# Kernel tuning notes

Measured on AMD Instinct MI355X. Metric: run time of the kernel, lower is better.

## Reference

```python
import jax, jax.numpy as jnp
import numpy as np

E = 20    # number of residue types (rc.restypes)
NB = 2    # num_blocks per AngleHead
NA = 7    # num_angles
C_S = 384
C_H = 128
BS, L = 8, 2048


def setup_inputs() -> dict:
    key = jax.random.key(0)
    ks = jax.random.split(key, 16)
    sc = 0.02
    return {
        "s": jax.random.normal(ks[0], (BS, L, C_S), dtype=jnp.float32),
        "s_init": jax.random.normal(ks[1], (BS, L, C_S), dtype=jnp.float32),
        "aatype": jax.random.randint(ks[2], (BS, L), 0, E, dtype=jnp.int32),
        # stacked per-residue-type AngleHead params
        "Win": jax.random.normal(ks[3], (E, C_S, C_H), dtype=jnp.float32) * sc,
        "b_in": jax.random.normal(ks[4], (E, C_H), dtype=jnp.float32) * sc,
        "Winit": jax.random.normal(ks[5], (E, C_S, C_H), dtype=jnp.float32) * sc,
        "b_init2": jax.random.normal(ks[6], (E, C_H), dtype=jnp.float32) * sc,
        "Wb1": jax.random.normal(ks[7], (E, NB, C_H, C_H), dtype=jnp.float32) * sc,
        "bb1": jax.random.normal(ks[8], (E, NB, C_H), dtype=jnp.float32) * sc,
        "Wb2": jax.random.normal(ks[9], (E, NB, C_H, C_H), dtype=jnp.float32) * sc,
        "bb2": jax.random.normal(ks[10], (E, NB, C_H), dtype=jnp.float32) * sc,
        "Wout": jax.random.normal(ks[11], (E, C_H, NA * 2), dtype=jnp.float32) * sc,
        "b_out": jax.random.normal(ks[12], (E, NA * 2), dtype=jnp.float32) * sc,
    }


def reference(s, s_init, aatype, Win, b_in, Winit, b_init2, Wb1, bb1, Wb2, bb2, Wout, b_out):
    relu = jax.nn.relu
    bs, seq_len, c_s = s.shape
    N = bs * seq_len
    sf = s.reshape(N, c_s)          # [N, c_s]
    si = s_init.reshape(N, c_s)     # [N, c_s]

    # Dense dispatch: run every token through all E per-type heads, then
    # combine with the one-hot routing mask (math identical to the torch
    # gather/scatter loop over residue types).
    h = jnp.einsum('nd,edh->neh', relu(sf), Win) + b_in            # [N,E,H]
    h = h + jnp.einsum('nd,edh->neh', relu(si), Winit) + b_init2   # [N,E,H]

    for b in range(NB):  # ResidualBlock1d: s + W2 @ relu(W1 @ relu(s))
        a = jnp.einsum('neh,ehk->nek', relu(h), Wb1[:, b]) + bb1[:, b]
        a = jnp.einsum('nek,ekh->neh', relu(a), Wb2[:, b]) + bb2[:, b]
        h = h + a

    out = jnp.einsum('neh,eho->neo', relu(h), Wout) + b_out        # [N,E,2*NA]
    sel = jax.nn.one_hot(aatype.reshape(N), E, dtype=out.dtype)    # [N,E]
    ang = jnp.einsum('neo,ne->no', out, sel).reshape(bs, seq_len, NA, 2)

    # F.normalize(dim=-1): x / max(||x||, eps)
    nrm = jnp.maximum(jnp.linalg.norm(ang, axis=-1, keepdims=True), 1e-12)
    return ang / nrm
```

## Files before the change

### kernel.cpp

```cpp
#include <hip/hip_runtime.h>
#include <math.h>

#define E_TYPES 20
#define NBLK 2
#define NANG 7
#define CS 384
#define CH 128
#define N_TOK (8 * 2048)
#define TOK 32
#define TPB 256
#define TPB_MAIN 512
#define KC 128
#define MAX_TILES (N_TOK / TOK + E_TYPES)
#define NPREP 64

#define HIST_OFF 0
#define CNT_OFF 1536
#define POFF_OFF 1600
#define PERM_OFF 2048

#define WT1_OFF (256 * 1024)
#define WT1_SZ  (20 * 8 * 24 * 2048)
#define WTR_OFF (WT1_OFF + WT1_SZ)

typedef __attribute__((ext_vector_type(8))) short bfrag;
typedef __attribute__((ext_vector_type(4))) float f32x4;

__device__ __forceinline__ void split_bf16(float x, unsigned short& h, unsigned short& l) {
    unsigned int u = __float_as_uint(x);
    unsigned int hb = (u + 0x7FFFu + ((u >> 16) & 1u)) & 0xFFFF0000u;
    h = (unsigned short)(hb >> 16);
    float r = x - __uint_as_float(hb);
    unsigned int v = __float_as_uint(r);
    l = (unsigned short)((v + 0x7FFFu + ((v >> 16) & 1u)) >> 16);
}

__global__ void prep1(const float* __restrict__ Win, const float* __restrict__ Winit,
                      const float* __restrict__ Wb1, const float* __restrict__ Wb2,
                      const int* __restrict__ aatype, int* __restrict__ wsI,
                      unsigned short* __restrict__ wt) {
    __shared__ int lh[E_TYPES];
    int bid = blockIdx.x;
    int t = threadIdx.x;
    if (bid >= 1600) {
        int b2 = bid - 1600;
        if (t < E_TYPES) lh[t] = 0;
        __syncthreads();
        int idx = b2 * 256 + t;
        if (idx < N_TOK) atomicAdd(&lh[aatype[idx]], 1);
        __syncthreads();
        if (t < E_TYPES) wsI[HIST_OFF + b2 * E_TYPES + t] = lh[t];
        return;
    }
    int gid = bid * 256 + t;
    unsigned short h[8], l[8];
    if (gid < 245760) {
        int lane = gid & 63;
        int bi = gid >> 6;
        int kb = bi % 24;
        int r = bi / 24;
        int nt = r & 7, e = r >> 3;
        int n = nt * 16 + (lane & 15);
        int k0 = kb * 32 + (lane >> 4) * 8;
        #pragma unroll
        for (int j = 0; j < 8; j++) {
            int k = k0 + j;
            float x = (k < CS) ? Win[((size_t)e * CS + k) * CH + n]
                               : Winit[((size_t)e * CS + (k - CS)) * CH + n];
            split_bf16(x, h[j], l[j]);
        }
        unsigned short* dst = wt + (WT1_OFF / 2) + (size_t)bi * 1024 + lane * 8;
        *(bfrag*)dst = *(bfrag*)h;
        *(bfrag*)(dst + 512) = *(bfrag*)l;
    } else {
        gid -= 245760;
        int lane = gid & 63;
        int bi = gid >> 6;
        int kb = bi & 3;
        int nt = (bi >> 2) & 7;
        int m4 = (bi >> 5) & 3;
        int e = bi >> 7;
        int b = m4 >> 1;
        const float* W = (m4 & 1) ? Wb2 : Wb1;
        int n = nt * 16 + (lane & 15);
        int k0 = kb * 32 + (lane >> 4) * 8;
        #pragma unroll
        for (int j = 0; j < 8; j++) {
            int k = k0 + j;
            float x = W[(((size_t)e * NBLK + b) * CH + k) * CH + n];
            split_bf16(x, h[j], l[j]);
        }
        unsigned short* dst = wt + (WTR_OFF / 2) + (size_t)bi * 1024 + lane * 8;
        *(bfrag*)dst = *(bfrag*)h;
        *(bfrag*)(dst + 512) = *(bfrag*)l;
    }
}

__global__ void scatter_k(const int* __restrict__ aatype, int* ws) {
    __shared__ int lhist[NPREP * E_TYPES];
    __shared__ int counts[E_TYPES], poff[E_TYPES + 1], mybase[E_TYPES], lcur[E_TYPES];
    int t = threadIdx.x;
    int bid = blockIdx.x;
    for (int idx = t; idx < NPREP * E_TYPES; idx += TPB)
        lhist[idx] = ws[HIST_OFF + idx];
    if (t < E_TYPES) lcur[t] = 0;
    __syncthreads();
    if (t < E_TYPES) {
        int tot = 0, pre = 0;
        for (int b = 0; b < NPREP; b++) {
            int v = lhist[b * E_TYPES + t];
            tot += v;
            if (b < bid) pre += v;
        }
        counts[t] = tot;
        mybase[t] = pre;
    }
    __syncthreads();
    if (t == 0) {
        int off = 0;
        for (int e = 0; e < E_TYPES; e++) {
            poff[e] = off;
            off += (counts[e] + TOK - 1) & ~(TOK - 1);
        }
        poff[E_TYPES] = off;
    }
    __syncthreads();
    if (t < E_TYPES) mybase[t] += poff[t];
    __syncthreads();
    int idx = bid * blockDim.x + t;
    if (idx < N_TOK) {
        int e = aatype[idx];
        int r = atomicAdd(&lcur[e], 1);
        ws[PERM_OFF + mybase[e] + r] = idx;
    }
    if (bid == 0) {
        if (t < E_TYPES) ws[CNT_OFF + t] = counts[t];
        if (t == 0)
            for (int e = 0; e <= E_TYPES; e++) ws[POFF_OFF + e] = poff[e];
    }
}

#define MFMA(a, b, c) __builtin_amdgcn_mfma_f32_16x16x32_bf16((a), (b), (c), 0, 0, 0)

__global__ __launch_bounds__(TPB_MAIN)
void angle_main(const float* __restrict__ s, const float* __restrict__ si,
                const float* __restrict__ b_in, const float* __restrict__ b_init2,
                const float* __restrict__ bb1, const float* __restrict__ bb2,
                const float* __restrict__ Wout, const float* __restrict__ b_out,
                const int* __restrict__ wsI, const unsigned short* __restrict__ wt,
                float* __restrict__ out)
{
    __shared__ unsigned short Ah[TOK][136];
    __shared__ unsigned short Al[TOK][136];
    __shared__ float Hf[TOK][132];
    __shared__ float Of[TOK][16];
    __shared__ int ptok[TOK];

    int pos = blockIdx.x * TOK;
    if (pos >= wsI[POFF_OFF + E_TYPES]) return;
    int e = 0;
    while (e < E_TYPES - 1 && pos >= wsI[POFF_OFF + e + 1]) e++;
    int n = wsI[CNT_OFF + e] - (pos - wsI[POFF_OFF + e]);
    if (n > TOK) n = TOK;

    int t = threadIdx.x;
    if (t < TOK) ptok[t] = wsI[PERM_OFF + pos + ((t < n) ? t : 0)];

    int w = t >> 6, lane = t & 63;
    int lane15 = lane & 15, quad = lane >> 4;
    int nc = w * 16 + lane15;

    const bfrag* wt1 = (const bfrag*)((const char*)wt + WT1_OFF);
    const bfrag* wtr = (const bfrag*)((const char*)wt + WTR_OFF);

    f32x4 acc[2];
    {
        float bv = b_in[e * CH + nc] + b_init2[e * CH + nc];
        acc[0] = (f32x4){bv, bv, bv, bv};
        acc[1] = acc[0];
    }

    __syncthreads();

    int srow = t >> 4;
    int scol = (t & 15) * 8;
    size_t rowoff = (size_t)ptok[srow] * CS + scol;
    float4 p0 = *(const float4*)(s + rowoff);
    float4 p1 = *(const float4*)(s + rowoff + 4);

    for (int c = 0; c < 6; c++) {
        {
            float xv[8] = {p0.x, p0.y, p0.z, p0.w, p1.x, p1.y, p1.z, p1.w};
            unsigned short h8[8], l8[8];
            #pragma unroll
            for (int j = 0; j < 8; j++)
                split_bf16(fmaxf(xv[j], 0.f), h8[j], l8[j]);
            *(bfrag*)&Ah[srow][scol] = *(bfrag*)h8;
            *(bfrag*)&Al[srow][scol] = *(bfrag*)l8;
        }
        __syncthreads();
        if (c < 5) {
            const float* src = (c + 1 < 3) ? s : si;
            int kb0 = ((c + 1 < 3) ? (c + 1) : (c - 2)) * KC;
            p0 = *(const float4*)(src + rowoff + kb0);
            p1 = *(const float4*)(src + rowoff + kb0 + 4);
        }
        #pragma unroll
        for (int ks = 0; ks < 4; ks++) {
            int kb = c * 4 + ks;
            int kl = ks * 32 + quad * 8;
            bfrag ah0 = *(const bfrag*)&Ah[lane15][kl];
            bfrag ah1 = *(const bfrag*)&Ah[16 + lane15][kl];
            bfrag al0 = *(const bfrag*)&Al[lane15][kl];
            bfrag al1 = *(const bfrag*)&Al[16 + lane15][kl];
            size_t b0 = ((size_t)(e * 8 + w) * 24 + kb) * 128;
            bfrag bh = wt1[b0 + lane];
            bfrag bl = wt1[b0 + 64 + lane];
            acc[0] = MFMA(ah0, bh, acc[0]);
            acc[0] = MFMA(ah0, bl, acc[0]);
            acc[0] = MFMA(al0, bh, acc[0]);
            acc[1] = MFMA(ah1, bh, acc[1]);
            acc[1] = MFMA(ah1, bl, acc[1]);
            acc[1] = MFMA(al1, bh, acc[1]);
        }
        __syncthreads();
    }

    for (int b = 0; b < NBLK; b++) {
        #pragma unroll
        for (int mt = 0; mt < 2; mt++) {
            f32x4 v = acc[mt];
            #pragma unroll
            for (int r = 0; r < 4; r++) {
                int m = mt * 16 + quad * 4 + r;
                unsigned short hh, ll;
                split_bf16(fmaxf(v[r], 0.f), hh, ll);
                Ah[m][nc] = hh;
                Al[m][nc] = ll;
            }
        }
        __syncthreads();

        f32x4 a2[2];
        {
            float bv = bb1[(e * NBLK + b) * CH + nc];
            a2[0] = (f32x4){bv, bv, bv, bv};
            a2[1] = a2[0];
        }
        #pragma unroll
        for (int ks = 0; ks < 4; ks++) {
            int kl = ks * 32 + quad * 8;
            bfrag ah0 = *(const bfrag*)&Ah[lane15][kl];
            bfrag ah1 = *(const bfrag*)&Ah[16 + lane15][kl];
            bfrag al0 = *(const bfrag*)&Al[lane15][kl];
            bfrag al1 = *(const bfrag*)&Al[16 + lane15][kl];
            size_t b0 = (((size_t)(e * 4 + 2 * b) * 8 + w) * 4 + ks) * 128;
            bfrag bh = wtr[b0 + lane], bl = wtr[b0 + 64 + lane];
            a2[0] = MFMA(ah0, bh, a2[0]);
            a2[0] = MFMA(ah0, bl, a2[0]);
            a2[0] = MFMA(al0, bh, a2[0]);
            a2[1] = MFMA(ah1, bh, a2[1]);
            a2[1] = MFMA(ah1, bl, a2[1]);
            a2[1] = MFMA(al1, bh, a2[1]);
        }
        __syncthreads();

        #pragma unroll
        for (int mt = 0; mt < 2; mt++) {
            f32x4 v = a2[mt];
            #pragma unroll
            for (int r = 0; r < 4; r++) {
                int m = mt * 16 + quad * 4 + r;
                unsigned short hh, ll;
                split_bf16(fmaxf(v[r], 0.f), hh, ll);
                Ah[m][nc] = hh;
                Al[m][nc] = ll;
            }
        }
        __syncthreads();

        f32x4 a3[2];
        {
            float bv = bb2[(e * NBLK + b) * CH + nc];
            a3[0] = (f32x4){bv, bv, bv, bv};
            a3[1] = a3[0];
        }
        #pragma unroll
        for (int ks = 0; ks < 4; ks++) {
            int kl = ks * 32 + quad * 8;
            bfrag ah0 = *(const bfrag*)&Ah[lane15][kl];
            bfrag ah1 = *(const bfrag*)&Ah[16 + lane15][kl];
            bfrag al0 = *(const bfrag*)&Al[lane15][kl];
            bfrag al1 = *(const bfrag*)&Al[16 + lane15][kl];
            size_t b0 = (((size_t)(e * 4 + 2 * b + 1) * 8 + w) * 4 + ks) * 128;
            bfrag bh = wtr[b0 + lane], bl = wtr[b0 + 64 + lane];
            a3[0] = MFMA(ah0, bh, a3[0]);
            a3[0] = MFMA(ah0, bl, a3[0]);
            a3[0] = MFMA(al0, bh, a3[0]);
            a3[1] = MFMA(ah1, bh, a3[1]);
            a3[1] = MFMA(ah1, bl, a3[1]);
            a3[1] = MFMA(al1, bh, a3[1]);
        }
        acc[0] += a3[0];
        acc[1] += a3[1];
        __syncthreads();
    }

    #pragma unroll
    for (int mt = 0; mt < 2; mt++) {
        f32x4 v = acc[mt];
        #pragma unroll
        for (int r = 0; r < 4; r++)
            Hf[mt * 16 + quad * 4 + r][nc] = fmaxf(v[r], 0.f);
    }
    __syncthreads();

    const float* WoutE = Wout + (size_t)e * CH * (NANG * 2);
    const float* boutE = b_out + (size_t)e * (NANG * 2);
    for (int idx = t; idx < n * (NANG * 2); idx += TPB_MAIN) {
        int i = idx / (NANG * 2);
        int o = idx - i * (NANG * 2);
        float v0 = boutE[o], v1 = 0.f, v2 = 0.f, v3 = 0.f;
        #pragma unroll 4
        for (int k = 0; k < CH; k += 4) {
            v0 = fmaf(Hf[i][k],     WoutE[(size_t)k * (NANG * 2) + o],       v0);
            v1 = fmaf(Hf[i][k + 1], WoutE[(size_t)(k + 1) * (NANG * 2) + o], v1);
            v2 = fmaf(Hf[i][k + 2], WoutE[(size_t)(k + 2) * (NANG * 2) + o], v2);
            v3 = fmaf(Hf[i][k + 3], WoutE[(size_t)(k + 3) * (NANG * 2) + o], v3);
        }
        Of[i][o] = (v0 + v1) + (v2 + v3);
    }
    __syncthreads();

    for (int idx = t; idx < n * NANG; idx += TPB_MAIN) {
        int i = idx / NANG;
        int a = idx - i * NANG;
        float x = Of[i][2 * a];
        float y = Of[i][2 * a + 1];
        float nr = fmaxf(sqrtf(x * x + y * y), 1e-12f);
        size_t base = (size_t)ptok[i] * (NANG * 2) + 2 * a;
        out[base]     = x / nr;
        out[base + 1] = y / nr;
    }
}

extern "C" void kernel_launch(void* const* d_in, const int* in_sizes, int n_in,
                              void* d_out, int out_size, void* d_ws, size_t ws_size,
                              hipStream_t stream) {
    const float* s       = (const float*)d_in[0];
    const float* s_init  = (const float*)d_in[1];
    const int*   aatype  = (const int*)d_in[2];
    const float* Win     = (const float*)d_in[3];
    const float* b_in    = (const float*)d_in[4];
    const float* Winit   = (const float*)d_in[5];
    const float* b_init2 = (const float*)d_in[6];
    const float* Wb1     = (const float*)d_in[7];
    const float* bb1     = (const float*)d_in[8];
    const float* Wb2     = (const float*)d_in[9];
    const float* bb2     = (const float*)d_in[10];
    const float* Wout    = (const float*)d_in[11];
    const float* b_out   = (const float*)d_in[12];
    int* wsI = (int*)d_ws;
    unsigned short* wt = (unsigned short*)d_ws;
    float* out = (float*)d_out;

    hipLaunchKernelGGL(prep1, dim3(1664), dim3(256), 0, stream,
                       Win, Winit, Wb1, Wb2, aatype, wsI, wt);
    hipLaunchKernelGGL(scatter_k, dim3(NPREP), dim3(TPB), 0, stream, aatype, wsI);
    hipLaunchKernelGGL(angle_main, dim3(MAX_TILES), dim3(TPB_MAIN), 0, stream,
                       s, s_init, b_in, b_init2, bb1, bb2, Wout, b_out,
                       wsI, wt, out);
}
```

Baseline: 160.0 us.

## Fuse token scatter into main kernel with double-buffered LDS and weight prefetch

Removes the separate scatter kernel. Each main block now rebuilds its tile's token list from the histogram with a wave-level prefix scan over aatype. The LDS activation buffers are double-buffered so one barrier per stage can be dropped, and the next weight fragments are prefetched into registers before they are needed. Block IDs are also remapped for XCD-aware tile assignment. This saves a kernel launch and some barriers, but every block now does redundant histogram and aatype scanning.

New measurement: 155.6 us. 2.8% less time.

```diff
diff --git a/kernel.cpp b/kernel.cpp
--- a/kernel.cpp
+++ b/kernel.cpp
@@ -15,9 +15,6 @@
 #define NPREP 64
 
 #define HIST_OFF 0
-#define CNT_OFF 1536
-#define POFF_OFF 1600
-#define PERM_OFF 2048
 
 #define WT1_OFF (256 * 1024)
 #define WT1_SZ  (20 * 8 * 24 * 2048)
@@ -25,6 +22,7 @@
 
 typedef __attribute__((ext_vector_type(8))) short bfrag;
 typedef __attribute__((ext_vector_type(4))) float f32x4;
+typedef unsigned short (*arr136)[136];
 
 __device__ __forceinline__ void split_bf16(float x, unsigned short& h, unsigned short& l) {
     unsigned int u = __float_as_uint(x);
@@ -96,50 +94,6 @@
     }
 }
 
-__global__ void scatter_k(const int* __restrict__ aatype, int* ws) {
-    __shared__ int lhist[NPREP * E_TYPES];
-    __shared__ int counts[E_TYPES], poff[E_TYPES + 1], mybase[E_TYPES], lcur[E_TYPES];
-    int t = threadIdx.x;
-    int bid = blockIdx.x;
-    for (int idx = t; idx < NPREP * E_TYPES; idx += TPB)
-        lhist[idx] = ws[HIST_OFF + idx];
-    if (t < E_TYPES) lcur[t] = 0;
-    __syncthreads();
-    if (t < E_TYPES) {
-        int tot = 0, pre = 0;
-        for (int b = 0; b < NPREP; b++) {
-            int v = lhist[b * E_TYPES + t];
-            tot += v;
-            if (b < bid) pre += v;
-        }
-        counts[t] = tot;
-        mybase[t] = pre;
-    }
-    __syncthreads();
-    if (t == 0) {
-        int off = 0;
-        for (int e = 0; e < E_TYPES; e++) {
-            poff[e] = off;
-            off += (counts[e] + TOK - 1) & ~(TOK - 1);
-        }
-        poff[E_TYPES] = off;
-    }
-    __syncthreads();
-    if (t < E_TYPES) mybase[t] += poff[t];
-    __syncthreads();
-    int idx = bid * blockDim.x + t;
-    if (idx < N_TOK) {
-        int e = aatype[idx];
-        int r = atomicAdd(&lcur[e], 1);
-        ws[PERM_OFF + mybase[e] + r] = idx;
-    }
-    if (bid == 0) {
-        if (t < E_TYPES) ws[CNT_OFF + t] = counts[t];
-        if (t == 0)
-            for (int e = 0; e <= E_TYPES; e++) ws[POFF_OFF + e] = poff[e];
-    }
-}
-
 #define MFMA(a, b, c) __builtin_amdgcn_mfma_f32_16x16x32_bf16((a), (b), (c), 0, 0, 0)
 
 __global__ __launch_bounds__(TPB_MAIN)
@@ -147,29 +101,88 @@
                 const float* __restrict__ b_in, const float* __restrict__ b_init2,
                 const float* __restrict__ bb1, const float* __restrict__ bb2,
                 const float* __restrict__ Wout, const float* __restrict__ b_out,
+                const int* __restrict__ aatype,
                 const int* __restrict__ wsI, const unsigned short* __restrict__ wt,
                 float* __restrict__ out)
 {
-    __shared__ unsigned short Ah[TOK][136];
-    __shared__ unsigned short Al[TOK][136];
-    __shared__ float Hf[TOK][132];
-    __shared__ float Of[TOK][16];
+    #define BUFSZ 17408
+    __shared__ __align__(16) char pool[2 * BUFSZ];
     __shared__ int ptok[TOK];
-
-    int pos = blockIdx.x * TOK;
-    if (pos >= wsI[POFF_OFF + E_TYPES]) return;
-    int e = 0;
-    while (e < E_TYPES - 1 && pos >= wsI[POFF_OFF + e + 1]) e++;
-    int n = wsI[CNT_OFF + e] - (pos - wsI[POFF_OFF + e]);
-    if (n > TOK) n = TOK;
+    __shared__ int cntS[E_TYPES];
+
+    arr136 AH0 = (arr136)(pool);
+    arr136 AL0 = (arr136)(pool + 8704);
+    arr136 AH1 = (arr136)(pool + BUFSZ);
+    arr136 AL1 = (arr136)(pool + BUFSZ + 8704);
+    float (*Hf)[132] = (float (*)[132])(pool);
+    float (*Of)[16]  = (float (*)[16])(pool + BUFSZ);
 
     int t = threadIdx.x;
-    if (t < TOK) ptok[t] = wsI[PERM_OFF + pos + ((t < n) ? t : 0)];
-
     int w = t >> 6, lane = t & 63;
     int lane15 = lane & 15, quad = lane >> 4;
+
+    int bid = blockIdx.x;
+    const int q = MAX_TILES >> 3, r = MAX_TILES & 7;
+    int xcd = bid & 7, sub = bid >> 3;
+    int tile = (xcd < r ? xcd * (q + 1) : r * (q + 1) + (xcd - r) * q) + sub;
+
+    if (w == 0 && lane < E_TYPES) {
+        int c = 0;
+        #pragma unroll
+        for (int b = 0; b < NPREP; b++) c += wsI[HIST_OFF + b * E_TYPES + lane];
+        cntS[lane] = c;
+    }
+    __syncthreads();
+
+    int pos = tile * TOK;
+    int e = -1, poff_e = 0;
+    {
+        int acc = 0;
+        #pragma unroll
+        for (int ee = 0; ee < E_TYPES; ee++) {
+            int pad = (cntS[ee] + TOK - 1) & ~(TOK - 1);
+            if (e < 0 && pos < acc + pad) { e = ee; poff_e = acc; }
+            acc += pad;
+        }
+        if (pos >= acc) return;
+    }
+    int pos_in = pos - poff_e;
+    int cnt_e = cntS[e];
+    int n = cnt_e - pos_in; if (n > TOK) n = TOK;
+
+    if (w == 0) {
+        int hb = wsI[HIST_OFF + lane * E_TYPES + e];
+        int inc = hb;
+        #pragma unroll
+        for (int d = 1; d < 64; d <<= 1) { int v = __shfl_up(inc, d); if (lane >= d) inc += v; }
+        int pre = inc - hb;
+        unsigned long long mle = __ballot(pre <= pos_in);
+        int cb = 63 - __clzll(mle);
+        int running = __shfl(pre, cb);
+        int base = cb * 256;
+        int lim = pos_in + n;
+        while (running < lim && base < N_TOK) {
+            const int4 a4 = *(const int4*)&aatype[base + lane * 4];
+            int m0 = (a4.x == e), m1 = (a4.y == e), m2 = (a4.z == e), m3 = (a4.w == e);
+            int c = m0 + m1 + m2 + m3;
+            int incl = c;
+            #pragma unroll
+            for (int d = 1; d < 64; d <<= 1) { int v = __shfl_up(incl, d); if (lane >= d) incl += v; }
+            int rk = running + incl - c;
+            int tk = base + lane * 4;
+            if (m0) { if (rk >= pos_in && rk < lim) ptok[rk - pos_in] = tk;     rk++; }
+            if (m1) { if (rk >= pos_in && rk < lim) ptok[rk - pos_in] = tk + 1; rk++; }
+            if (m2) { if (rk >= pos_in && rk < lim) ptok[rk - pos_in] = tk + 2; rk++; }
+            if (m3) { if (rk >= pos_in && rk < lim) ptok[rk - pos_in] = tk + 3; rk++; }
+            running += __shfl(incl, 63);
+            base += 256;
+        }
+        int t0 = ptok[0];
+        if (lane >= n && lane < TOK) ptok[lane] = t0;
+    }
+    __syncthreads();
+
     int nc = w * 16 + lane15;
-
     const bfrag* wt1 = (const bfrag*)((const char*)wt + WT1_OFF);
     const bfrag* wtr = (const bfrag*)((const char*)wt + WTR_OFF);
 
@@ -180,42 +193,45 @@
         acc[1] = acc[0];
     }
 
-    __syncthreads();
-
     int srow = t >> 4;
     int scol = (t & 15) * 8;
     size_t rowoff = (size_t)ptok[srow] * CS + scol;
     float4 p0 = *(const float4*)(s + rowoff);
     float4 p1 = *(const float4*)(s + rowoff + 4);
-
+    size_t wb = (size_t)(e * 8 + w) * 24;
+    bfrag pbh = wt1[wb * 128 + lane];
+    bfrag pbl = wt1[wb * 128 + 64 + lane];
+
+    #pragma unroll
     for (int c = 0; c < 6; c++) {
+        arr136 WAH = (c & 1) ? AH1 : AH0;
+        arr136 WAL = (c & 1) ? AL1 : AL0;
         {
             float xv[8] = {p0.x, p0.y, p0.z, p0.w, p1.x, p1.y, p1.z, p1.w};
             unsigned short h8[8], l8[8];
             #pragma unroll
             for (int j = 0; j < 8; j++)
                 split_bf16(fmaxf(xv[j], 0.f), h8[j], l8[j]);
-            *(bfrag*)&Ah[srow][scol] = *(bfrag*)h8;
-            *(bfrag*)&Al[srow][scol] = *(bfrag*)l8;
-        }
-        __syncthreads();
+            *(bfrag*)&WAH[srow][scol] = *(bfrag*)h8;
+            *(bfrag*)&WAL[srow][scol] = *(bfrag*)l8;
+        }
         if (c < 5) {
             const float* src = (c + 1 < 3) ? s : si;
             int kb0 = ((c + 1 < 3) ? (c + 1) : (c - 2)) * KC;
             p0 = *(const float4*)(src + rowoff + kb0);
             p1 = *(const float4*)(src + rowoff + kb0 + 4);
         }
+        __syncthreads();
         #pragma unroll
         for (int ks = 0; ks < 4; ks++) {
             int kb = c * 4 + ks;
+            bfrag bh = ks ? wt1[(wb + kb) * 128 + lane]      : pbh;
+            bfrag bl = ks ? wt1[(wb + kb) * 128 + 64 + lane] : pbl;
             int kl = ks * 32 + quad * 8;
-            bfrag ah0 = *(const bfrag*)&Ah[lane15][kl];
-            bfrag ah1 = *(const bfrag*)&Ah[16 + lane15][kl];
-            bfrag al0 = *(const bfrag*)&Al[lane15][kl];
-            bfrag al1 = *(const bfrag*)&Al[16 + lane15][kl];
-            size_t b0 = ((size_t)(e * 8 + w) * 24 + kb) * 128;
-            bfrag bh = wt1[b0 + lane];
-            bfrag bl = wt1[b0 + 64 + lane];
+            bfrag ah0 = *(const bfrag*)&WAH[lane15][kl];
+            bfrag ah1 = *(const bfrag*)&WAH[16 + lane15][kl];
+            bfrag al0 = *(const bfrag*)&WAL[lane15][kl];
+            bfrag al1 = *(const bfrag*)&WAL[16 + lane15][kl];
             acc[0] = MFMA(ah0, bh, acc[0]);
             acc[0] = MFMA(ah0, bl, acc[0]);
             acc[0] = MFMA(al0, bh, acc[0]);
@@ -223,95 +239,69 @@
             acc[1] = MFMA(ah1, bl, acc[1]);
             acc[1] = MFMA(al1, bh, acc[1]);
         }
+        if (c < 5) {
+            pbh = wt1[(wb + (c + 1) * 4) * 128 + lane];
+            pbl = wt1[(wb + (c + 1) * 4) * 128 + 64 + lane];
+        }
+    }
+
+    {
+        size_t g0 = ((size_t)(e * 4) * 8 + w) * 4;
+        pbh = wtr[g0 * 128 + lane];
+        pbl = wtr[g0 * 128 + 64 + lane];
+    }
+    f32x4 cur[2] = {acc[0], acc[1]};
+    #pragma unroll
+    for (int g = 0; g < 4; g++) {
+        arr136 WAH = (g & 1) ? AH1 : AH0;
+        arr136 WAL = (g & 1) ? AL1 : AL0;
+        #pragma unroll
+        for (int mt = 0; mt < 2; mt++) {
+            f32x4 v = cur[mt];
+            #pragma unroll
+            for (int rr = 0; rr < 4; rr++) {
+                unsigned short hh, ll;
+                split_bf16(fmaxf(v[rr], 0.f), hh, ll);
+                WAH[mt * 16 + quad * 4 + rr][nc] = hh;
+                WAL[mt * 16 + quad * 4 + rr][nc] = ll;
+            }
+        }
         __syncthreads();
-    }
-
-    for (int b = 0; b < NBLK; b++) {
-        #pragma unroll
-        for (int mt = 0; mt < 2; mt++) {
-            f32x4 v = acc[mt];
-            #pragma unroll
-            for (int r = 0; r < 4; r++) {
-                int m = mt * 16 + quad * 4 + r;
-                unsigned short hh, ll;
-                split_bf16(fmaxf(v[r], 0.f), hh, ll);
-                Ah[m][nc] = hh;
-                Al[m][nc] = ll;
-            }
-        }
-        __syncthreads();
-
-        f32x4 a2[2];
-        {
-            float bv = bb1[(e * NBLK + b) * CH + nc];
-            a2[0] = (f32x4){bv, bv, bv, bv};
-            a2[1] = a2[0];
-        }
+        float bv = (g & 1) ? bb2[(e * NBLK + (g >> 1)) * CH + nc]
+                           : bb1[(e * NBLK + (g >> 1)) * CH + nc];
+        f32x4 r0 = (f32x4){bv, bv, bv, bv}, r1 = r0;
+        size_t wgb = ((size_t)(e * 4 + g) * 8 + w) * 4;
         #pragma unroll
         for (int ks = 0; ks < 4; ks++) {
+            bfrag bh = ks ? wtr[(wgb + ks) * 128 + lane]      : pbh;
+            bfrag bl = ks ? wtr[(wgb + ks) * 128 + 64 + lane] : pbl;
             int kl = ks * 32 + quad * 8;
-            bfrag ah0 = *(const bfrag*)&Ah[lane15][kl];
-            bfrag ah1 = *(const bfrag*)&Ah[16 + lane15][kl];
-            bfrag al0 = *(const bfrag*)&Al[lane15][kl];
-            bfrag al1 = *(const bfrag*)&Al[16 + lane15][kl];
-            size_t b0 = (((size_t)(e * 4 + 2 * b) * 8 + w) * 4 + ks) * 128;
-            bfrag bh = wtr[b0 + lane], bl = wtr[b0 + 64 + lane];
-            a2[0] = MFMA(ah0, bh, a2[0]);
-            a2[0] = MFMA(ah0, bl, a2[0]);
-            a2[0] = MFMA(al0, bh, a2[0]);
-            a2[1] = MFMA(ah1, bh, a2[1]);
-            a2[1] = MFMA(ah1, bl, a2[1]);
-            a2[1] = MFMA(al1, bh, a2[1]);
-        }
-        __syncthreads();
-
-        #pragma unroll
-        for (int mt = 0; mt < 2; mt++) {
-            f32x4 v = a2[mt];
-            #pragma unroll
-            for (int r = 0; r < 4; r++) {
-                int m = mt * 16 + quad * 4 + r;
-                unsigned short hh, ll;
-                split_bf16(fmaxf(v[r], 0.f), hh, ll);
-                Ah[m][nc] = hh;
-                Al[m][nc] = ll;
-            }
-        }
-        __syncthreads();
-
-        f32x4 a3[2];
-        {
-            float bv = bb2[(e * NBLK + b) * CH + nc];
-            a3[0] = (f32x4){bv, bv, bv, bv};
-            a3[1] = a3[0];
-        }
-        #pragma unroll
-        for (int ks = 0; ks < 4; ks++) {
-            int kl = ks * 32 + quad * 8;
-            bfrag ah0 = *(const bfrag*)&Ah[lane15][kl];
-            bfrag ah1 = *(const bfrag*)&Ah[16 + lane15][kl];
-            bfrag al0 = *(const bfrag*)&Al[lane15][kl];
-            bfrag al1 = *(const bfrag*)&Al[16 + lane15][kl];
-            size_t b0 = (((size_t)(e * 4 + 2 * b + 1) * 8 + w) * 4 + ks) * 128;
-            bfrag bh = wtr[b0 + lane], bl = wtr[b0 + 64 + lane];
-            a3[0] = MFMA(ah0, bh, a3[0]);
-            a3[0] = MFMA(ah0, bl, a3[0]);
-            a3[0] = MFMA(al0, bh, a3[0]);
-            a3[1] = MFMA(ah1, bh, a3[1]);
-            a3[1] = MFMA(ah1, bl, a3[1]);
-            a3[1] = MFMA(al1, bh, a3[1]);
-        }
-        acc[0] += a3[0];
-        acc[1] += a3[1];
-        __syncthreads();
+            bfrag ah0 = *(const bfrag*)&WAH[lane15][kl];
+            bfrag ah1 = *(const bfrag*)&WAH[16 + lane15][kl];
+            bfrag al0 = *(const bfrag*)&WAL[lane15][kl];
+            bfrag al1 = *(const bfrag*)&WAL[16 + lane15][kl];
+            r0 = MFMA(ah0, bh, r0);
+            r0 = MFMA(ah0, bl, r0);
+            r0 = MFMA(al0, bh, r0);
+            r1 = MFMA(ah1, bh, r1);
+            r1 = MFMA(ah1, bl, r1);
+            r1 = MFMA(al1, bh, r1);
+        }
+        if (g < 3) {
+            size_t nb = ((size_t)(e * 4 + g + 1) * 8 + w) * 4;
+            pbh = wtr[nb * 128 + lane];
+            pbl = wtr[nb * 128 + 64 + lane];
+        }
+        if (g & 1) { acc[0] += r0; acc[1] += r1; cur[0] = acc[0]; cur[1] = acc[1]; }
+        else       { cur[0] = r0; cur[1] = r1; }
     }
 
     #pragma unroll
     for (int mt = 0; mt < 2; mt++) {
         f32x4 v = acc[mt];
         #pragma unroll
-        for (int r = 0; r < 4; r++)
-            Hf[mt * 16 + quad * 4 + r][nc] = fmaxf(v[r], 0.f);
+        for (int rr = 0; rr < 4; rr++)
+            Hf[mt * 16 + quad * 4 + rr][nc] = fmaxf(v[rr], 0.f);
     }
     __syncthreads();
 
@@ -366,8 +356,7 @@
 
     hipLaunchKernelGGL(prep1, dim3(1664), dim3(256), 0, stream,
                        Win, Winit, Wb1, Wb2, aatype, wsI, wt);
-    hipLaunchKernelGGL(scatter_k, dim3(NPREP), dim3(TPB), 0, stream, aatype, wsI);
     hipLaunchKernelGGL(angle_main, dim3(MAX_TILES), dim3(TPB_MAIN), 0, stream,
                        s, s_init, b_in, b_init2, bb1, bb2, Wout, b_out,
-                       wsI, wt, out);
+                       aatype, wsI, wt, out);
 }
```
